# Performance work log

Hardware: AMD Instinct MI355X
Metric: run time of the kernel (lower is better)

Reference implementation:

```python
import jax, jax.numpy as jnp
import numpy as np

# ---- static config (matches torch module defaults) ----
SPATIAL = np.array([[100, 100], [50, 50], [25, 25], [13, 13]], dtype=np.int64)  # [L,2] (H,W)
EMBED, HEADS, LEVELS, POINTS = 256, 8, 4, 4
HEAD_DIM = EMBED // HEADS
TOTAL_POINTS = HEADS * LEVELS * POINTS
BS, LQ = 32, 300
LV = int((SPATIAL[:, 0] * SPATIAL[:, 1]).sum())  # 13294


def setup_inputs() -> dict:
    key = jax.random.key(0)
    ks = jax.random.split(key, 12)
    s = 1.0 / np.sqrt(EMBED)
    return {
        "query": jax.random.normal(ks[0], (BS, LQ, EMBED), jnp.float32),
        "reference_points": jax.random.uniform(ks[1], (BS, LQ, LEVELS, 2), jnp.float32),
        "value": jax.random.normal(ks[2], (BS, LV, EMBED), jnp.float32),
        "value_spatial_shapes": jnp.asarray(SPATIAL),
        # learned parameters (torch: Linear weight [out,in] -> stored here as [in,out])
        "W_off": jax.random.normal(ks[3], (EMBED, TOTAL_POINTS * 2), jnp.float32) * 0.01,
        "b_off": jax.random.normal(ks[4], (TOTAL_POINTS * 2,), jnp.float32) * 0.01,
        "W_attn": jax.random.normal(ks[5], (EMBED, TOTAL_POINTS), jnp.float32) * s,
        "b_attn": jnp.zeros((TOTAL_POINTS,), jnp.float32),
        "W_val": jax.random.normal(ks[6], (EMBED, EMBED), jnp.float32) * s,
        "b_val": jnp.zeros((EMBED,), jnp.float32),
        "W_out": jax.random.normal(ks[7], (EMBED, EMBED), jnp.float32) * s,
        "b_out": jnp.zeros((EMBED,), jnp.float32),
    }


def _bilinear_sample(v, grid, H, W):
    """F.grid_sample(mode='bilinear', padding_mode='zeros', align_corners=False).
    v: [H*W, c], grid: [Lq, P, 2] in [-1, 1] (x, y). Returns [Lq, P, c]."""
    x = (grid[..., 0] + 1.0) * 0.5 * W - 0.5
    y = (grid[..., 1] + 1.0) * 0.5 * H - 0.5
    x0f, y0f = jnp.floor(x), jnp.floor(y)
    lx, ly = x - x0f, y - y0f
    x0, y0 = x0f.astype(jnp.int32), y0f.astype(jnp.int32)

    def gather(iy, ix):
        valid = ((iy >= 0) & (iy < H) & (ix >= 0) & (ix < W)).astype(v.dtype)[..., None]
        idx = jnp.clip(iy, 0, H - 1) * W + jnp.clip(ix, 0, W - 1)
        return v[idx] * valid

    return (gather(y0, x0) * ((1 - ly) * (1 - lx))[..., None]
            + gather(y0, x0 + 1) * ((1 - ly) * lx)[..., None]
            + gather(y0 + 1, x0) * (ly * (1 - lx))[..., None]
            + gather(y0 + 1, x0 + 1) * (ly * lx)[..., None])


def _ms_deform_attn_core(value, sampling_grids, attention_weights):
    """value: [bs, Lv, H, c]; sampling_grids: [bs, Lq, H, L, P, 2] in [-1,1];
    attention_weights: [bs, Lq, H, L, P] -> output [bs, Lq, H*c]."""
    bs, Lq = sampling_grids.shape[:2]
    samples = []
    start = 0
    for lvl in range(LEVELS):
        H, W = int(SPATIAL[lvl, 0]), int(SPATIAL[lvl, 1])
        # [bs, HW, nh, c] -> [bs*nh, HW, c]
        v_l = value[:, start:start + H * W]
        v_l = v_l.transpose(0, 2, 1, 3).reshape(bs * HEADS, H * W, HEAD_DIM)
        # [bs, Lq, nh, P, 2] -> [bs*nh, Lq, P, 2]
        g_l = sampling_grids[:, :, :, lvl].transpose(0, 2, 1, 3, 4).reshape(bs * HEADS, Lq, POINTS, 2)
        samples.append(jax.vmap(lambda vv, gg: _bilinear_sample(vv, gg, H, W))(v_l, g_l))
        start += H * W
    stacked = jnp.stack(samples, axis=2)  # [bs*nh, Lq, L, P, c]
    aw = attention_weights.transpose(0, 2, 1, 3, 4).reshape(bs * HEADS, Lq, LEVELS, POINTS)
    out = (stacked * aw[..., None]).sum(axis=(2, 3))  # [bs*nh, Lq, c]
    return out.reshape(bs, HEADS, Lq, HEAD_DIM).transpose(0, 2, 1, 3).reshape(bs, Lq, EMBED)


def reference(query, reference_points, value, value_spatial_shapes,
              W_off, b_off, W_attn, b_attn, W_val, b_val, W_out, b_out):
    bs, Lq = query.shape[:2]
    Lv = value.shape[1]

    value_p = (value @ W_val + b_val).reshape(bs, Lv, HEADS, HEAD_DIM)

    offsets = (query @ W_off + b_off).reshape(bs, Lq, HEADS, LEVELS, POINTS, 2)
    attn = jax.nn.softmax((query @ W_attn + b_attn).reshape(bs, Lq, HEADS, LEVELS * POINTS), axis=-1)
    attn = attn.reshape(bs, Lq, HEADS, LEVELS, POINTS)

    # offset_normalizer = flip(spatial_shapes) -> (W, H) per level
    norm = jnp.asarray(SPATIAL[:, ::-1].copy(), jnp.float32)  # [L, 2]
    sampling_locations = (reference_points[:, :, None, :, None, :]
                          + offsets / norm[None, None, None, :, None, :])
    sampling_grids = 2.0 * sampling_locations - 1.0

    out = _ms_deform_attn_core(value_p, sampling_grids, attn)
    return out @ W_out + b_out
```

## Files before the change

kernel.cpp:

```cpp
#include <hip/hip_runtime.h>
#include <hip/hip_bf16.h>

#define BS_   32
#define LQ_   300
#define LV_   13294
#define EMBED_ 256
#define HEADS_ 8
#define HEAD_DIM_ 32
#define NCHUNK_ 13294
#define PSTRIDE_ 512

typedef __attribute__((ext_vector_type(8))) short bf16x8;
typedef __attribute__((ext_vector_type(4))) float f32x4;

__device__ inline short f2bf(float f) {
  union { float f; unsigned u; } x; x.f = f;
  return (short)((x.u + 0x7FFF + ((x.u >> 16) & 1)) >> 16);
}
__device__ inline short f2bf_i(float f) {
  union { __hip_bfloat16 h; short s; } u;
  u.h = __float2bfloat16(f);
  return u.s;
}
__device__ inline float bf2f(short s) {
  union { unsigned u; float f; } x; x.u = ((unsigned)(unsigned short)s) << 16;
  return x.f;
}

__device__ __forceinline__ void gld_lds16(const void* g, void* l) {
  __builtin_amdgcn_global_load_lds(
      (const __attribute__((address_space(1))) unsigned int*)g,
      (__attribute__((address_space(3))) unsigned int*)l, 16, 0, 0);
}

__global__ void convert_wt(const float* __restrict__ W, short* __restrict__ Wt,
                           int Nsrc) {
  const int n = blockIdx.x;
  const int k = threadIdx.x;
  Wt[n * 256 + k] = (n < Nsrc) ? f2bf(W[k * Nsrc + n]) : (short)0;
}

__global__ void convert_wq(const float* __restrict__ W_off,
                           const float* __restrict__ W_attn,
                           short* __restrict__ Wt) {
  const int n = blockIdx.x;
  const int k = threadIdx.x;
  Wt[n * 256 + k] = (n < 256) ? f2bf(W_off[k * 256 + n])
                              : f2bf(W_attn[k * 128 + (n - 256)]);
}

__global__ __launch_bounds__(512, 2) void gemm_value_persist(
    const float* __restrict__ A, const short* __restrict__ Wt,
    const float* __restrict__ bias, short* __restrict__ Vp) {
  __shared__ float As[2][32 * 256];

  const int tid = threadIdx.x;
  const int lane = tid & 63;
  const int w = tid >> 6;
  const int lr = lane & 15;
  const int lkq = lane >> 4;

  bf16x8 bfr[2][8];
#pragma unroll
  for (int nf = 0; nf < 2; ++nf) {
    const size_t bbase = (size_t)(w * 32 + nf * 16 + lr) * 256 + lkq * 8;
#pragma unroll
    for (int kt = 0; kt < 8; ++kt)
      bfr[nf][kt] = *(const bf16x8*)(Wt + bbase + kt * 32);
  }
  float bv[2];
#pragma unroll
  for (int nf = 0; nf < 2; ++nf) bv[nf] = bias[w * 32 + nf * 16 + lr];

  auto stage = [&](int buf, int c) {
    const float* src = A + (size_t)c * (32 * 256);
#pragma unroll
    for (int i = 0; i < 4; ++i) {
      const int r = w * 4 + i;
      gld_lds16(src + r * 256 + ((lane ^ (r & 7)) * 4), &As[buf][r * 256]);
    }
  };

  const int c0 = blockIdx.x;
  stage(0, c0);
  asm volatile("s_waitcnt vmcnt(0)" ::: "memory");
  __syncthreads();

  int cb = 0;
  for (int c = c0; c < NCHUNK_; c += PSTRIDE_) {
    const int nxt = c + PSTRIDE_;
    if (nxt < NCHUNK_) stage(cb ^ 1, nxt);

    f32x4 acc[2][2];
#pragma unroll
    for (int i = 0; i < 2; ++i)
#pragma unroll
      for (int jj = 0; jj < 2; ++jj) acc[i][jj] = (f32x4){0.f, 0.f, 0.f, 0.f};

    const float* as = &As[cb][0];
#pragma unroll
    for (int kt = 0; kt < 8; ++kt) {
      const int r0 = lr;
      const int r1 = 16 + lr;
      const int g = kt * 8 + lkq * 2;
      const f32x4 a00 = *(const f32x4*)(as + r0 * 256 + (((g    ) ^ (r0 & 7)) * 4));
      const f32x4 a01 = *(const f32x4*)(as + r0 * 256 + (((g + 1) ^ (r0 & 7)) * 4));
      const f32x4 a10 = *(const f32x4*)(as + r1 * 256 + (((g    ) ^ (r1 & 7)) * 4));
      const f32x4 a11 = *(const f32x4*)(as + r1 * 256 + (((g + 1) ^ (r1 & 7)) * 4));
      bf16x8 af0, af1;
#pragma unroll
      for (int i = 0; i < 4; ++i) {
        af0[i]     = f2bf_i(a00[i]);
        af0[i + 4] = f2bf_i(a01[i]);
        af1[i]     = f2bf_i(a10[i]);
        af1[i + 4] = f2bf_i(a11[i]);
      }
      acc[0][0] = __builtin_amdgcn_mfma_f32_16x16x32_bf16(af0, bfr[0][kt], acc[0][0], 0, 0, 0);
      acc[0][1] = __builtin_amdgcn_mfma_f32_16x16x32_bf16(af0, bfr[1][kt], acc[0][1], 0, 0, 0);
      acc[1][0] = __builtin_amdgcn_mfma_f32_16x16x32_bf16(af1, bfr[0][kt], acc[1][0], 0, 0, 0);
      acc[1][1] = __builtin_amdgcn_mfma_f32_16x16x32_bf16(af1, bfr[1][kt], acc[1][1], 0, 0, 0);
    }

#pragma unroll
    for (int mf = 0; mf < 2; ++mf)
#pragma unroll
      for (int rr = 0; rr < 4; ++rr) {
        const unsigned m = (unsigned)c * 32 + mf * 16 + lkq * 4 + rr;
        const unsigned b_ = m / LV_;
        const unsigned pos = m - b_ * LV_;
        const size_t rowbase = ((size_t)(b_ * HEADS_ + w) * LV_ + pos) * HEAD_DIM_;
#pragma unroll
        for (int nf = 0; nf < 2; ++nf)
          Vp[rowbase + nf * 16 + lr] = f2bf(acc[mf][nf][rr] + bv[nf]);
      }

    if (nxt < NCHUNK_) {
      asm volatile("s_waitcnt vmcnt(16)" ::: "memory");
      asm volatile("s_barrier" ::: "memory");
    }
    cb ^= 1;
  }
}

__global__ __launch_bounds__(384, 2) void gemm_qproj2(
    const float* __restrict__ A, const short* __restrict__ Wt,
    const float* __restrict__ b_off, const float* __restrict__ b_attn,
    float* __restrict__ offs, float* __restrict__ logits) {
  __shared__ float As[64 * 256];

  const int tid = threadIdx.x;
  const int lane = tid & 63;
  const int w = tid >> 6;
  const int n0 = w * 64;
  const size_t m0 = (size_t)blockIdx.x * 64;
  const int lr = lane & 15;
  const int lkq = lane >> 4;

  if (w < 4) {
#pragma unroll
    for (int i = 0; i < 16; ++i) {
      const int row = w * 16 + i;
      gld_lds16(A + (m0 + row) * 256 + ((lane ^ (row & 7)) * 4), As + row * 256);
    }
  }

  bf16x8 bfr[4][8];
#pragma unroll
  for (int nf = 0; nf < 4; ++nf) {
    const size_t bbase = (size_t)(n0 + nf * 16 + lr) * 256 + lkq * 8;
#pragma unroll
    for (int kt = 0; kt < 8; ++kt)
      bfr[nf][kt] = *(const bf16x8*)(Wt + bbase + kt * 32);
  }

  f32x4 acc[4][4];
#pragma unroll
  for (int i = 0; i < 4; ++i)
#pragma unroll
    for (int jj = 0; jj < 4; ++jj) acc[i][jj] = (f32x4){0.f, 0.f, 0.f, 0.f};

  __syncthreads();

#pragma unroll
  for (int kt = 0; kt < 8; ++kt) {
#pragma unroll
    for (int mf = 0; mf < 4; ++mf) {
      const int row = mf * 16 + lr;
      const int gbase = kt * 8 + lkq * 2;
      const f32x4 a0 = *(const f32x4*)(As + row * 256 + ((gbase) ^ (row & 7)) * 4);
      const f32x4 a1 = *(const f32x4*)(As + row * 256 + ((gbase + 1) ^ (row & 7)) * 4);
      bf16x8 af;
#pragma unroll
      for (int i = 0; i < 4; ++i) {
        af[i]     = f2bf_i(a0[i]);
        af[i + 4] = f2bf_i(a1[i]);
      }
#pragma unroll
      for (int nf = 0; nf < 4; ++nf)
        acc[mf][nf] = __builtin_amdgcn_mfma_f32_16x16x32_bf16(af, bfr[nf][kt], acc[mf][nf], 0, 0, 0);
    }
  }

  float bv[4];
#pragma unroll
  for (int nf = 0; nf < 4; ++nf) {
    const int n = n0 + nf * 16 + lr;
    bv[nf] = (n < 256) ? b_off[n] : b_attn[n - 256];
  }
  const int lq4 = lkq * 4;
#pragma unroll
  for (int mf = 0; mf < 4; ++mf)
#pragma unroll
    for (int r = 0; r < 4; ++r) {
      const size_t m = m0 + mf * 16 + lq4 + r;
#pragma unroll
      for (int nf = 0; nf < 4; ++nf) {
        const int n = n0 + nf * 16 + lr;
        if (n < 256) offs[m * 256 + n] = acc[mf][nf][r] + bv[nf];
        else         logits[m * 128 + (n - 256)] = acc[mf][nf][r] + bv[nf];
      }
    }
}

__global__ __launch_bounds__(256, 2) void gemm_qproj(
    const float* __restrict__ A, const short* __restrict__ Wt,
    const float* __restrict__ bias, float* __restrict__ C) {
  __shared__ float As[64 * 256];

  const int tid = threadIdx.x;
  const int lane = tid & 63;
  const int w = tid >> 6;
  const int n0 = w * 64;
  const size_t m0 = (size_t)blockIdx.x * 64;
  const int lr = lane & 15;
  const int lkq = lane >> 4;

#pragma unroll
  for (int i = 0; i < 16; ++i) {
    const int row = w * 16 + i;
    gld_lds16(A + (m0 + row) * 256 + ((lane ^ (row & 7)) * 4), As + row * 256);
  }

  bf16x8 bfr[4][8];
#pragma unroll
  for (int nf = 0; nf < 4; ++nf) {
    const size_t bbase = (size_t)(n0 + nf * 16 + lr) * 256 + lkq * 8;
#pragma unroll
    for (int kt = 0; kt < 8; ++kt)
      bfr[nf][kt] = *(const bf16x8*)(Wt + bbase + kt * 32);
  }

  f32x4 acc[4][4];
#pragma unroll
  for (int i = 0; i < 4; ++i)
#pragma unroll
    for (int jj = 0; jj < 4; ++jj) acc[i][jj] = (f32x4){0.f, 0.f, 0.f, 0.f};

  __syncthreads();

#pragma unroll
  for (int kt = 0; kt < 8; ++kt) {
#pragma unroll
    for (int mf = 0; mf < 4; ++mf) {
      const int row = mf * 16 + lr;
      const int gbase = kt * 8 + lkq * 2;
      const f32x4 a0 = *(const f32x4*)(As + row * 256 + ((gbase) ^ (row & 7)) * 4);
      const f32x4 a1 = *(const f32x4*)(As + row * 256 + ((gbase + 1) ^ (row & 7)) * 4);
      bf16x8 af;
#pragma unroll
      for (int i = 0; i < 4; ++i) {
        af[i]     = f2bf_i(a0[i]);
        af[i + 4] = f2bf_i(a1[i]);
      }
#pragma unroll
      for (int nf = 0; nf < 4; ++nf)
        acc[mf][nf] = __builtin_amdgcn_mfma_f32_16x16x32_bf16(af, bfr[nf][kt], acc[mf][nf], 0, 0, 0);
    }
  }

  float bv[4];
#pragma unroll
  for (int nf = 0; nf < 4; ++nf) bv[nf] = bias[n0 + nf * 16 + lr];
  const int lq4 = lkq * 4;
#pragma unroll
  for (int mf = 0; mf < 4; ++mf)
#pragma unroll
    for (int r = 0; r < 4; ++r) {
      const size_t m = m0 + mf * 16 + lq4 + r;
#pragma unroll
      for (int nf = 0; nf < 4; ++nf) {
        const int n = n0 + nf * 16 + lr;
        C[m * 256 + n] = acc[mf][nf][r] + bv[nf];
      }
    }
}

__global__ __launch_bounds__(256) void msda_sample_fused(
    const float* __restrict__ ref_pts,
    const float* __restrict__ offsets,
    const float* __restrict__ logits,
    const short* __restrict__ value_p,
    float* __restrict__ tmp)
{
  const int t = blockIdx.x * 256 + threadIdx.x;
  const int c16 = t & 1;
  const int h = (t >> 1) & 7;
  const int row = t >> 4;
  const int b = row / LQ_;

  const int HS[4] = {100, 50, 25, 13};
  const int START[4] = {0, 10000, 12500, 13125};

  const float* lg = logits + (size_t)row * 128 + h * 16;
  float wv[16];
  float mx = -1e30f;
#pragma unroll
  for (int i = 0; i < 4; ++i) {
    const f32x4 v = *(const f32x4*)(lg + i * 4);
#pragma unroll
    for (int jj = 0; jj < 4; ++jj) { wv[i * 4 + jj] = v[jj]; mx = fmaxf(mx, v[jj]); }
  }
  float sum = 0.f;
#pragma unroll
  for (int i = 0; i < 16; ++i) { wv[i] = __expf(wv[i] - mx); sum += wv[i]; }
  const float inv = 1.0f / sum;
#pragma unroll
  for (int i = 0; i < 16; ++i) wv[i] *= inv;

  const float* offr = offsets + (size_t)row * 256 + h * 32;
  const float* refr = ref_pts + (size_t)row * 8;

  float acc[16];
#pragma unroll
  for (int jj = 0; jj < 16; ++jj) acc[jj] = 0.f;

#pragma unroll
  for (int l = 0; l < 4; ++l) {
    const int HH = HS[l];
    const int WW = HS[l];
    const float fH = (float)HH, fW = (float)WW;
    const float rx = refr[l * 2 + 0];
    const float ry = refr[l * 2 + 1];
    const short* vbase =
        value_p + ((size_t)(b * HEADS_ + h) * LV_ + START[l]) * HEAD_DIM_ + c16 * 16;
#pragma unroll
    for (int p = 0; p < 4; ++p) {
      const float ox = offr[(l * 4 + p) * 2 + 0];
      const float oy = offr[(l * 4 + p) * 2 + 1];
      const float x = (rx + ox / fW) * fW - 0.5f;
      const float y = (ry + oy / fH) * fH - 0.5f;
      const float x0f = floorf(x), y0f = floorf(y);
      const float fx = x - x0f, fy = y - y0f;
      const int x0 = (int)x0f, y0 = (int)y0f;
      const float wgt = wv[l * 4 + p];
      const float iy0 = (y0 >= 0 && y0 < HH) ? 1.f : 0.f;
      const float iy1 = (y0 + 1 >= 0 && y0 + 1 < HH) ? 1.f : 0.f;
      const float ix0 = (x0 >= 0 && x0 < WW) ? 1.f : 0.f;
      const float ix1 = (x0 + 1 >= 0 && x0 + 1 < WW) ? 1.f : 0.f;
      const float w00 = (1.f - fy) * (1.f - fx) * wgt * iy0 * ix0;
      const float w01 = (1.f - fy) * fx * wgt * iy0 * ix1;
      const float w10 = fy * (1.f - fx) * wgt * iy1 * ix0;
      const float w11 = fy * fx * wgt * iy1 * ix1;
      const int xc0 = min(max(x0, 0), WW - 1);
      const int xc1 = min(max(x0 + 1, 0), WW - 1);
      const int yc0 = min(max(y0, 0), HH - 1);
      const int yc1 = min(max(y0 + 1, 0), HH - 1);
      const short* p00 = vbase + (size_t)(yc0 * WW + xc0) * HEAD_DIM_;
      const short* p01 = vbase + (size_t)(yc0 * WW + xc1) * HEAD_DIM_;
      const short* p10 = vbase + (size_t)(yc1 * WW + xc0) * HEAD_DIM_;
      const short* p11 = vbase + (size_t)(yc1 * WW + xc1) * HEAD_DIM_;
      const bf16x8 q00a = *(const bf16x8*)(p00);
      const bf16x8 q00b = *(const bf16x8*)(p00 + 8);
      const bf16x8 q01a = *(const bf16x8*)(p01);
      const bf16x8 q01b = *(const bf16x8*)(p01 + 8);
      const bf16x8 q10a = *(const bf16x8*)(p10);
      const bf16x8 q10b = *(const bf16x8*)(p10 + 8);
      const bf16x8 q11a = *(const bf16x8*)(p11);
      const bf16x8 q11b = *(const bf16x8*)(p11 + 8);
#pragma unroll
      for (int jj = 0; jj < 8; ++jj) {
        acc[jj] += w00 * bf2f(q00a[jj]) + w01 * bf2f(q01a[jj]) +
                   w10 * bf2f(q10a[jj]) + w11 * bf2f(q11a[jj]);
        acc[jj + 8] += w00 * bf2f(q00b[jj]) + w01 * bf2f(q01b[jj]) +
                       w10 * bf2f(q10b[jj]) + w11 * bf2f(q11b[jj]);
      }
    }
  }
  float* o = tmp + (size_t)row * 256 + h * 32 + c16 * 16;
#pragma unroll
  for (int i = 0; i < 4; ++i) {
    f32x4 v = {acc[i * 4], acc[i * 4 + 1], acc[i * 4 + 2], acc[i * 4 + 3]};
    *(f32x4*)(o + i * 4) = v;
  }
}

extern "C" void kernel_launch(void* const* d_in, const int* in_sizes, int n_in,
                              void* d_out, int out_size, void* d_ws, size_t ws_size,
                              hipStream_t stream) {
  const float* query  = (const float*)d_in[0];
  const float* refpts = (const float*)d_in[1];
  const float* value  = (const float*)d_in[2];
  const float* W_off  = (const float*)d_in[4];
  const float* b_off  = (const float*)d_in[5];
  const float* W_attn = (const float*)d_in[6];
  const float* b_attn = (const float*)d_in[7];
  const float* W_val  = (const float*)d_in[8];
  const float* b_val  = (const float*)d_in[9];
  const float* W_out  = (const float*)d_in[10];
  const float* b_out  = (const float*)d_in[11];
  float* out = (float*)d_out;

  char* ws = (char*)d_ws;
  short* value_p = (short*)ws;
  size_t off = (size_t)BS_ * HEADS_ * LV_ * HEAD_DIM_ * 2;
  float* offsets = (float*)(ws + off); off += (size_t)BS_ * LQ_ * 256 * 4;
  float* logits  = (float*)(ws + off); off += (size_t)BS_ * LQ_ * 128 * 4;
  float* tmp     = (float*)(ws + off); off += (size_t)BS_ * LQ_ * 256 * 4;

  short* WtQ = (short*)value_p;
  short* WtV = (short*)tmp;
  short* WtO = (short*)value_p;

  const int MQ = BS_ * LQ_;

  convert_wq<<<384, 256, 0, stream>>>(W_off, W_attn, WtQ);
  gemm_qproj2<<<MQ / 64, 384, 0, stream>>>(query, WtQ, b_off, b_attn, offsets, logits);
  convert_wt<<<256, 256, 0, stream>>>(W_val, WtV, 256);
  gemm_value_persist<<<PSTRIDE_, 512, 0, stream>>>(value, WtV, b_val, value_p);
  msda_sample_fused<<<(MQ * 16) / 256, 256, 0, stream>>>(refpts, offsets, logits, value_p, tmp);
  convert_wt<<<256, 256, 0, stream>>>(W_out, WtO, 256);
  gemm_qproj<<<MQ / 64, 256, 0, stream>>>(tmp, WtO, b_out, out);
}
```

Baseline: 242.9 us.

## Merge weight conversions into one launch and split sampling across 4 lanes per head

The three weight-transpose/convert kernels become a single launch that writes into dedicated workspace buffers rather than reusing the value_p and tmp regions, which removes two launches. The sampling kernel now assigns 8 channels per thread (4 threads per head) instead of 16, doubling the thread count. This gives more parallelism and fewer registers per thread for the latency-bound gathers. The cost is that the softmax and coordinate math are now repeated across twice as many threads.

```diff
diff --git a/kernel.cpp b/kernel.cpp
--- a/kernel.cpp
+++ b/kernel.cpp
@@ -33,20 +33,23 @@
       (__attribute__((address_space(3))) unsigned int*)l, 16, 0, 0);
 }
 
-__global__ void convert_wt(const float* __restrict__ W, short* __restrict__ Wt,
-                           int Nsrc) {
+__global__ void convert_all(const float* __restrict__ W_off,
+                            const float* __restrict__ W_attn,
+                            const float* __restrict__ W_val,
+                            const float* __restrict__ W_out,
+                            short* __restrict__ WtQ,
+                            short* __restrict__ WtV,
+                            short* __restrict__ WtO) {
   const int n = blockIdx.x;
   const int k = threadIdx.x;
-  Wt[n * 256 + k] = (n < Nsrc) ? f2bf(W[k * Nsrc + n]) : (short)0;
-}
-
-__global__ void convert_wq(const float* __restrict__ W_off,
-                           const float* __restrict__ W_attn,
-                           short* __restrict__ Wt) {
-  const int n = blockIdx.x;
-  const int k = threadIdx.x;
-  Wt[n * 256 + k] = (n < 256) ? f2bf(W_off[k * 256 + n])
-                              : f2bf(W_attn[k * 128 + (n - 256)]);
+  if (n < 384) {
+    WtQ[n * 256 + k] = (n < 256) ? f2bf(W_off[k * 256 + n])
+                                 : f2bf(W_attn[k * 128 + (n - 256)]);
+  } else if (n < 640) {
+    WtV[(n - 384) * 256 + k] = f2bf(W_val[k * 256 + (n - 384)]);
+  } else {
+    WtO[(n - 640) * 256 + k] = f2bf(W_out[k * 256 + (n - 640)]);
+  }
 }
 
 __global__ __launch_bounds__(512, 2) void gemm_value_persist(
@@ -303,9 +306,9 @@
     float* __restrict__ tmp)
 {
   const int t = blockIdx.x * 256 + threadIdx.x;
-  const int c16 = t & 1;
-  const int h = (t >> 1) & 7;
-  const int row = t >> 4;
+  const int c8 = t & 3;
+  const int h = (t >> 2) & 7;
+  const int row = t >> 5;
   const int b = row / LQ_;
 
   const int HS[4] = {100, 50, 25, 13};
@@ -330,9 +333,9 @@
   const float* offr = offsets + (size_t)row * 256 + h * 32;
   const float* refr = ref_pts + (size_t)row * 8;
 
-  float acc[16];
-#pragma unroll
-  for (int jj = 0; jj < 16; ++jj) acc[jj] = 0.f;
+  float acc[8];
+#pragma unroll
+  for (int jj = 0; jj < 8; ++jj) acc[jj] = 0.f;
 
 #pragma unroll
   for (int l = 0; l < 4; ++l) {
@@ -342,7 +345,7 @@
     const float rx = refr[l * 2 + 0];
     const float ry = refr[l * 2 + 1];
     const short* vbase =
-        value_p + ((size_t)(b * HEADS_ + h) * LV_ + START[l]) * HEAD_DIM_ + c16 * 16;
+        value_p + ((size_t)(b * HEADS_ + h) * LV_ + START[l]) * HEAD_DIM_ + c8 * 8;
 #pragma unroll
     for (int p = 0; p < 4; ++p) {
       const float ox = offr[(l * 4 + p) * 2 + 0];
@@ -365,33 +368,22 @@
       const int xc1 = min(max(x0 + 1, 0), WW - 1);
       const int yc0 = min(max(y0, 0), HH - 1);
       const int yc1 = min(max(y0 + 1, 0), HH - 1);
-      const short* p00 = vbase + (size_t)(yc0 * WW + xc0) * HEAD_DIM_;
-      const short* p01 = vbase + (size_t)(yc0 * WW + xc1) * HEAD_DIM_;
-      const short* p10 = vbase + (size_t)(yc1 * WW + xc0) * HEAD_DIM_;
-      const short* p11 = vbase + (size_t)(yc1 * WW + xc1) * HEAD_DIM_;
-      const bf16x8 q00a = *(const bf16x8*)(p00);
-      const bf16x8 q00b = *(const bf16x8*)(p00 + 8);
-      const bf16x8 q01a = *(const bf16x8*)(p01);
-      const bf16x8 q01b = *(const bf16x8*)(p01 + 8);
-      const bf16x8 q10a = *(const bf16x8*)(p10);
-      const bf16x8 q10b = *(const bf16x8*)(p10 + 8);
-      const bf16x8 q11a = *(const bf16x8*)(p11);
-      const bf16x8 q11b = *(const bf16x8*)(p11 + 8);
+      const bf16x8 q00 = *(const bf16x8*)(vbase + (size_t)(yc0 * WW + xc0) * HEAD_DIM_);
+      const bf16x8 q01 = *(const bf16x8*)(vbase + (size_t)(yc0 * WW + xc1) * HEAD_DIM_);
+      const bf16x8 q10 = *(const bf16x8*)(vbase + (size_t)(yc1 * WW + xc0) * HEAD_DIM_);
+      const bf16x8 q11 = *(const bf16x8*)(vbase + (size_t)(yc1 * WW + xc1) * HEAD_DIM_);
 #pragma unroll
       for (int jj = 0; jj < 8; ++jj) {
-        acc[jj] += w00 * bf2f(q00a[jj]) + w01 * bf2f(q01a[jj]) +
-                   w10 * bf2f(q10a[jj]) + w11 * bf2f(q11a[jj]);
-        acc[jj + 8] += w00 * bf2f(q00b[jj]) + w01 * bf2f(q01b[jj]) +
-                       w10 * bf2f(q10b[jj]) + w11 * bf2f(q11b[jj]);
-      }
-    }
-  }
-  float* o = tmp + (size_t)row * 256 + h * 32 + c16 * 16;
-#pragma unroll
-  for (int i = 0; i < 4; ++i) {
-    f32x4 v = {acc[i * 4], acc[i * 4 + 1], acc[i * 4 + 2], acc[i * 4 + 3]};
-    *(f32x4*)(o + i * 4) = v;
-  }
+        acc[jj] += w00 * bf2f(q00[jj]) + w01 * bf2f(q01[jj]) +
+                   w10 * bf2f(q10[jj]) + w11 * bf2f(q11[jj]);
+      }
+    }
+  }
+  float* o = tmp + (size_t)row * 256 + h * 32 + c8 * 8;
+  f32x4 o0 = {acc[0], acc[1], acc[2], acc[3]};
+  f32x4 o1 = {acc[4], acc[5], acc[6], acc[7]};
+  *(f32x4*)(o) = o0;
+  *(f32x4*)(o + 4) = o1;
 }
 
 extern "C" void kernel_launch(void* const* d_in, const int* in_sizes, int n_in,
@@ -416,18 +408,15 @@
   float* offsets = (float*)(ws + off); off += (size_t)BS_ * LQ_ * 256 * 4;
   float* logits  = (float*)(ws + off); off += (size_t)BS_ * LQ_ * 128 * 4;
   float* tmp     = (float*)(ws + off); off += (size_t)BS_ * LQ_ * 256 * 4;
-
-  short* WtQ = (short*)value_p;
-  short* WtV = (short*)tmp;
-  short* WtO = (short*)value_p;
+  short* WtQ = (short*)(ws + off); off += 384 * 256 * 2;
+  short* WtV = (short*)(ws + off); off += 256 * 256 * 2;
+  short* WtO = (short*)(ws + off); off += 256 * 256 * 2;
 
   const int MQ = BS_ * LQ_;
 
-  convert_wq<<<384, 256, 0, stream>>>(W_off, W_attn, WtQ);
+  convert_all<<<896, 256, 0, stream>>>(W_off, W_attn, W_val, W_out, WtQ, WtV, WtO);
   gemm_qproj2<<<MQ / 64, 384, 0, stream>>>(query, WtQ, b_off, b_attn, offsets, logits);
-  convert_wt<<<256, 256, 0, stream>>>(W_val, WtV, 256);
   gemm_value_persist<<<PSTRIDE_, 512, 0, stream>>>(value, WtV, b_val, value_p);
-  msda_sample_fused<<<(MQ * 16) / 256, 256, 0, stream>>>(refpts, offsets, logits, value_p, tmp);
-  convert_wt<<<256, 256, 0, stream>>>(W_out, WtO, 256);
+  msda_sample_fused<<<(MQ * 32) / 256, 256, 0, stream>>>(refpts, offsets, logits, value_p, tmp);
   gemm_qproj<<<MQ / 64, 256, 0, stream>>>(tmp, WtO, b_out, out);
 }
```

Result: faster. 210.8 us (-13.2%).
